# Kernel tuning notes

Hardware: AMD Instinct MI355X
Metric: run time of the kernel (lower is better)

Reference implementation:

```python
import jax, jax.numpy as jnp
import numpy as np

N_NODES = 100000
N_EDGES = 1600000
IN_DIM = 256
HIDDEN = 128
N_CLASSES = 40


def gcn_conv(x, W, b, src, dst, n_nodes):
    """torch_geometric GCNConv: transform -> add self-loops -> sym-normalized sum-aggregate -> +bias."""
    h = x @ W  # [N, out]
    loop = jnp.arange(n_nodes, dtype=src.dtype)
    src2 = jnp.concatenate([src, loop])
    dst2 = jnp.concatenate([dst, loop])
    # degree with self-loops (edge weight 1)
    deg = jax.ops.segment_sum(jnp.ones_like(dst2, dtype=h.dtype), dst2, num_segments=n_nodes)
    dinv = jnp.where(deg > 0, jax.lax.rsqrt(deg), 0.0)
    norm = dinv[src2] * dinv[dst2]  # [E+N]
    msg = h[src2] * norm[:, None]   # [E+N, out] gather + scale
    out = jax.ops.segment_sum(msg, dst2, num_segments=n_nodes)
    return out + b


def setup_inputs() -> dict:
    key = jax.random.key(0)
    k1, k2, k3, k4 = jax.random.split(key, 4)
    x = jax.random.normal(k1, (N_NODES, IN_DIM), dtype=jnp.float32)
    edge_index = jax.random.randint(k2, (2, N_EDGES), 0, N_NODES, dtype=jnp.int64)
    W1 = jax.random.normal(k3, (IN_DIM, HIDDEN), dtype=jnp.float32) * (1.0 / np.sqrt(IN_DIM))
    b1 = jnp.zeros((HIDDEN,), dtype=jnp.float32)
    W2 = jax.random.normal(k4, (HIDDEN, N_CLASSES), dtype=jnp.float32) * (1.0 / np.sqrt(HIDDEN))
    b2 = jnp.zeros((N_CLASSES,), dtype=jnp.float32)
    return {"x": x, "edge_index": edge_index, "W1": W1, "b1": b1, "W2": W2, "b2": b2}


def reference(x, edge_index, W1, b1, W2, b2):
    src, dst = edge_index[0], edge_index[1]
    h = gcn_conv(x, W1, b1, src, dst, N_NODES)
    h = jax.nn.relu(h)
    # dropout p=0.5 is identity in eval mode
    out = gcn_conv(h, W2, b2, src, dst, N_NODES)
    return out
```

## Files before the change

### kernel.cpp

```cpp
#include <hip/hip_runtime.h>
#include <hip/hip_bf16.h>
#include <hip/hip_fp16.h>

#define N_NODES 100000
#define N_EDGES 1600000
#define IN_DIM 256
#define HIDDEN 128
#define NCLS 40
#define NCLS_PAD 48

#define N_BUCKETS 256
#define NPB 391
#define BCAP 8192
#define EPT 16
#define BIN_WG 4096
#define BIN_BLOCKS 391
#define GEMM1_BLOCKS 782

typedef __attribute__((ext_vector_type(8))) _Float16 half8;
typedef __attribute__((ext_vector_type(4))) _Float16 half4f;
typedef __attribute__((ext_vector_type(4))) float floatx4;


__global__ __launch_bounds__(256) void k_prep(const float* __restrict__ W1, __half* __restrict__ W1T,
                                              const float* __restrict__ W2, __half* __restrict__ W2T,
                                              int* __restrict__ bfill) {
    const int t = threadIdx.x;
    if (blockIdx.x < 128) {
        int i = blockIdx.x * 256 + t;
        int k = i >> 7, n = i & 127;
        W1T[n * IN_DIM + k] = __float2half_rn(W1[i]);
    } else if (blockIdx.x == 128) {
        for (int i = t; i < NCLS_PAD * HIDDEN; i += 256) {
            int n = i >> 7, k = i & 127;
            W2T[n * HIDDEN + k] = (n < NCLS) ? __float2half_rn(W2[k * NCLS + n]) : __float2half_rn(0.f);
        }
    } else {
        bfill[t] = 0;
    }
}


__global__ __launch_bounds__(256) void k_binmm(const int* __restrict__ src, const int* __restrict__ dst,
                                               int* __restrict__ bfill,
                                               unsigned long long* __restrict__ bpair,
                                               const float* __restrict__ X,
                                               const __half* __restrict__ W1T,
                                               __half* __restrict__ H1s) {
    __shared__ __align__(16) char smraw[39936];
    const int t = threadIdx.x;

    if (blockIdx.x < BIN_BLOCKS) {
        int* hist   = (int*)smraw;
        int* bstart = hist + 256;
        int* gbase  = bstart + 256;
        unsigned long long* stage = (unsigned long long*)(smraw + 3072);
        unsigned char* bid = (unsigned char*)(smraw + 3072 + 32768);
        hist[t] = 0;
        __syncthreads();
        const long e0 = (long)blockIdx.x * BIN_WG;
        const int n_valid = (int)min((long)BIN_WG, (long)N_EDGES - e0);
        int msrc[EPT], mdst[EPT], moff[EPT];
        #pragma unroll
        for (int i = 0; i < EPT; i++) {
            long e = e0 + t + i * 256;
            if (e < N_EDGES) {
                msrc[i] = src[e];
                mdst[i] = dst[e];
                moff[i] = atomicAdd(&hist[mdst[i] / NPB], 1);
            } else {
                mdst[i] = -1;
            }
        }
        __syncthreads();
        if (t < 64) {
            int carry = 0;
            #pragma unroll
            for (int c = 0; c < 4; c++) {
                int idx = c * 64 + t;
                int hv = hist[idx];
                int s = hv;
                #pragma unroll
                for (int d2 = 1; d2 < 64; d2 <<= 1) {
                    int u = __shfl_up(s, d2, 64);
                    if (t >= d2) s += u;
                }
                bstart[idx] = carry + (s - hv);
                carry += __shfl(s, 63, 64);
            }
        }
        __syncthreads();
        int h = hist[t];
        gbase[t] = (h > 0) ? atomicAdd(&bfill[t], h) : 0;
        #pragma unroll
        for (int i = 0; i < EPT; i++) {
            if (mdst[i] >= 0) {
                int b = mdst[i] / NPB;
                int pos = bstart[b] + moff[i];
                stage[pos] = ((unsigned long long)(unsigned)mdst[i] << 32) | (unsigned)msrc[i];
                bid[pos] = (unsigned char)b;
            }
        }
        __syncthreads();
        for (int i = t; i < n_valid; i += 256) {
            int b = bid[i];
            int dest = gbase[b] + (i - bstart[b]);
            bpair[(long)b * BCAP + dest] = stage[i];
        }
        return;
    }

    _Float16 (*Asm)[72] = (_Float16(*)[72])smraw;
    _Float16 (*Bsm)[72] = (_Float16(*)[72])(smraw + 128 * 72 * 2);
    const int wave = t >> 6;
    const int lane = t & 63;
    const int m16  = lane & 15;
    const int kq   = lane >> 4;
    const int row0 = (blockIdx.x - BIN_BLOCKS) * 128;

    floatx4 acc[2][8];
    #pragma unroll
    for (int mt = 0; mt < 2; mt++)
        #pragma unroll
        for (int i = 0; i < 8; i++) acc[mt][i] = (floatx4)0.f;

    float4 ar[4][2];
    auto loadA = [&](int kcL) {
        #pragma unroll
        for (int it = 0; it < 4; it++) {
            int u = t + it * 256;
            int r = u >> 3, j = u & 7;
            int gr = row0 + r;
            if (gr < N_NODES) {
                const float* p = &X[(long)gr * IN_DIM + kcL * 64 + j * 8];
                ar[it][0] = *(const float4*)p;
                ar[it][1] = *(const float4*)(p + 4);
            } else {
                ar[it][0] = make_float4(0.f, 0.f, 0.f, 0.f);
                ar[it][1] = make_float4(0.f, 0.f, 0.f, 0.f);
            }
        }
    };

    loadA(0);
    for (int kc = 0; kc < 4; kc++) {
        #pragma unroll
        for (int it = 0; it < 4; it++) {
            int u = t + it * 256;
            int r = u >> 3, j = u & 7;
            half8 hh;
            hh[0] = (_Float16)ar[it][0].x; hh[1] = (_Float16)ar[it][0].y;
            hh[2] = (_Float16)ar[it][0].z; hh[3] = (_Float16)ar[it][0].w;
            hh[4] = (_Float16)ar[it][1].x; hh[5] = (_Float16)ar[it][1].y;
            hh[6] = (_Float16)ar[it][1].z; hh[7] = (_Float16)ar[it][1].w;
            *(half8*)&Asm[r][j * 8] = hh;
        }
        #pragma unroll
        for (int it = 0; it < 4; it++) {
            int u = t + it * 256;
            int n = u >> 3, j = u & 7;
            float4 w = *(const float4*)&W1T[n * IN_DIM + kc * 64 + j * 8];
            *(float4*)&Bsm[n][j * 8] = w;
        }
        __syncthreads();
        if (kc < 3) loadA(kc + 1);
        #pragma unroll
        for (int ks = 0; ks < 2; ks++) {
            half8 a0 = *(const half8*)&Asm[wave * 32 + m16][ks * 32 + kq * 8];
            half8 a1 = *(const half8*)&Asm[wave * 32 + 16 + m16][ks * 32 + kq * 8];
            #pragma unroll
            for (int nt = 0; nt < 8; nt++) {
                half8 b = *(const half8*)&Bsm[nt * 16 + m16][ks * 32 + kq * 8];
                acc[0][nt] = __builtin_amdgcn_mfma_f32_16x16x32_f16(a0, b, acc[0][nt], 0, 0, 0);
                acc[1][nt] = __builtin_amdgcn_mfma_f32_16x16x32_f16(a1, b, acc[1][nt], 0, 0, 0);
            }
        }
        __syncthreads();
    }
    #pragma unroll
    for (int mt = 0; mt < 2; mt++) {
        const int gr0 = row0 + wave * 32 + mt * 16 + kq * 4;
        #pragma unroll
        for (int nt = 0; nt < 8; nt++) {
            int c = nt * 16 + m16;
            #pragma unroll
            for (int r = 0; r < 4; r++) {
                if (gr0 + r < N_NODES)
                    H1s[(long)(gr0 + r) * HIDDEN + c] = __float2half_rn(acc[mt][nt][r]);
            }
        }
    }
}


__global__ __launch_bounds__(256) void k_build(const int* __restrict__ bfill,
                                               const unsigned long long* __restrict__ bpair,
                                               int* __restrict__ row_ptr, float* __restrict__ dinv,
                                               int* __restrict__ col) {
    __shared__ int h[NPB];
    __shared__ int pfx[NPB];
    __shared__ int sred[4];
    const int b  = blockIdx.x;
    const int nb = b * NPB;
    const int nn = min(NPB, N_NODES - nb);
    const int t  = threadIdx.x;
    int v = (t < b) ? bfill[t] : 0;
    #pragma unroll
    for (int dl = 32; dl > 0; dl >>= 1) v += __shfl_down(v, dl, 64);
    if ((t & 63) == 0) sred[t >> 6] = v;
    for (int i = t; i < NPB; i += 256) h[i] = 0;
    __syncthreads();
    const int base_b = sred[0] + sred[1] + sred[2] + sred[3];
    const int n = bfill[b];
    for (int i = t; i < n; i += 256) {
        int dd = (int)(bpair[(long)b * BCAP + i] >> 32);
        atomicAdd(&h[dd - nb], 1);
    }
    __syncthreads();
    if (t < 64) {
        int carry = 0;
        #pragma unroll
        for (int c = 0; c < (NPB + 63) / 64; c++) {
            int idx = c * 64 + t;
            int hv = (idx < nn) ? h[idx] : 0;
            int s = hv;
            #pragma unroll
            for (int d2 = 1; d2 < 64; d2 <<= 1) {
                int u = __shfl_up(s, d2, 64);
                if (t >= d2) s += u;
            }
            if (idx < nn) {
                int ex = base_b + carry + (s - hv);
                pfx[idx] = ex;
                row_ptr[nb + idx] = ex;
                dinv[nb + idx] = rsqrtf((float)(hv + 1));
            }
            carry += __shfl(s, 63, 64);
        }
    }
    __syncthreads();
    for (int i = t; i < nn; i += 256) h[i] = 0;
    __syncthreads();
    for (int i = t; i < n; i += 256) {
        unsigned long long p = bpair[(long)b * BCAP + i];
        int dd = (int)(p >> 32);
        int ss = (int)(p & 0xFFFFFFFFu);
        int pos = pfx[dd - nb] + atomicAdd(&h[dd - nb], 1);
        col[pos] = ss;
    }
    if (b == 0 && t == 0) row_ptr[N_NODES] = N_EDGES;
}


__global__ __launch_bounds__(256) void k_agg1g2(const __half* __restrict__ H1s,
                                                const int* __restrict__ row_ptr,
                                                const int* __restrict__ col,
                                                const float* __restrict__ dinv,
                                                const float* __restrict__ b1,
                                                const __half* __restrict__ W2T,
                                                __half* __restrict__ H2s) {
    __shared__ __align__(16) _Float16 rows[16][136];
    const int wave = threadIdx.x >> 6;
    const int lane = threadIdx.x & 63;
    const __half2* base = (const __half2*)H1s;
    const float2 bb = ((const float2*)b1)[lane];
    const int d00 = blockIdx.x * 16 + wave * 4;

    #pragma unroll
    for (int i = 0; i < 4; i++) {
        const int d = d00 + i;
        const int e0 = __builtin_amdgcn_readfirstlane(row_ptr[d]);
        const int e1 = __builtin_amdgcn_readfirstlane(row_ptr[d + 1]);
        const float dd = dinv[d];
        float ax = 0.f, ay = 0.f;
        int e = e0;
        for (; e + 7 < e1; e += 8) {
            int s0 = col[e],     s1 = col[e + 1], s2 = col[e + 2], s3 = col[e + 3];
            int s4 = col[e + 4], s5 = col[e + 5], s6 = col[e + 6], s7 = col[e + 7];
            float d0 = dinv[s0], d1 = dinv[s1], d2 = dinv[s2], d3 = dinv[s3];
            float d4 = dinv[s4], d5 = dinv[s5], d6 = dinv[s6], d7 = dinv[s7];
            float2 f0 = __half22float2(base[(long)s0 * 64 + lane]);
            float2 f1 = __half22float2(base[(long)s1 * 64 + lane]);
            float2 f2 = __half22float2(base[(long)s2 * 64 + lane]);
            float2 f3 = __half22float2(base[(long)s3 * 64 + lane]);
            float2 f4 = __half22float2(base[(long)s4 * 64 + lane]);
            float2 f5 = __half22float2(base[(long)s5 * 64 + lane]);
            float2 f6 = __half22float2(base[(long)s6 * 64 + lane]);
            float2 f7 = __half22float2(base[(long)s7 * 64 + lane]);
            ax += d0 * f0.x + d1 * f1.x + d2 * f2.x + d3 * f3.x
                + d4 * f4.x + d5 * f5.x + d6 * f6.x + d7 * f7.x;
            ay += d0 * f0.y + d1 * f1.y + d2 * f2.y + d3 * f3.y
                + d4 * f4.y + d5 * f5.y + d6 * f6.y + d7 * f7.y;
        }
        for (; e + 3 < e1; e += 4) {
            int s0 = col[e], s1 = col[e + 1], s2 = col[e + 2], s3 = col[e + 3];
            float d0 = dinv[s0], d1 = dinv[s1], d2 = dinv[s2], d3 = dinv[s3];
            float2 f0 = __half22float2(base[(long)s0 * 64 + lane]);
            float2 f1 = __half22float2(base[(long)s1 * 64 + lane]);
            float2 f2 = __half22float2(base[(long)s2 * 64 + lane]);
            float2 f3 = __half22float2(base[(long)s3 * 64 + lane]);
            ax += d0 * f0.x + d1 * f1.x + d2 * f2.x + d3 * f3.x;
            ay += d0 * f0.y + d1 * f1.y + d2 * f2.y + d3 * f3.y;
        }
        for (; e < e1; e++) {
            int s = col[e];
            float dv = dinv[s];
            float2 f = __half22float2(base[(long)s * 64 + lane]);
            ax += dv * f.x; ay += dv * f.y;
        }
        float2 fs = __half22float2(base[(long)d * 64 + lane]);
        ax += dd * fs.x; ay += dd * fs.y;
        float ox = fmaxf(dd * ax + bb.x, 0.f) * dd;
        float oy = fmaxf(dd * ay + bb.y, 0.f) * dd;
        *(__half2*)&rows[wave * 4 + i][lane * 2] =
            __halves2half2(__float2half_rn(ox), __float2half_rn(oy));
    }
    __syncthreads();

    if (wave < 3) {
        const int m16 = lane & 15;
        const int kq  = lane >> 4;
        floatx4 acc = (floatx4)0.f;
        #pragma unroll
        for (int ks = 0; ks < 4; ks++) {
            half8 a = *(const half8*)&rows[m16][ks * 32 + kq * 8];
            half8 b = *(const half8*)&W2T[(wave * 16 + m16) * HIDDEN + ks * 32 + kq * 8];
            acc = __builtin_amdgcn_mfma_f32_16x16x32_f16(a, b, acc, 0, 0, 0);
        }
        const int c = wave * 16 + m16;
        if (c < NCLS) {
            const int gr0 = blockIdx.x * 16 + kq * 4;
            #pragma unroll
            for (int r = 0; r < 4; r++)
                H2s[(long)(gr0 + r) * NCLS + c] = __float2half_rn(acc[r]);
        }
    }
}


__global__ __launch_bounds__(256) void k_agg2(const __half* __restrict__ H2s,
                                              const int* __restrict__ row_ptr,
                                              const int* __restrict__ col,
                                              const float* __restrict__ dinv,
                                              const float* __restrict__ b2,
                                              float* __restrict__ out) {
    const int wave = threadIdx.x >> 6;
    const int lane = threadIdx.x & 63;
    const int g = lane / 10;
    const int f = lane - g * 10;
    const int d = blockIdx.x * 24 + wave * 6 + g;
    const bool act = (g < 6) && (d < N_NODES);
    int e0 = 0, e1 = 0;
    if (act) { e0 = row_ptr[d]; e1 = row_ptr[d + 1]; }
    const half4f* base4 = (const half4f*)H2s;
    float s0 = 0.f, s1 = 0.f, s2 = 0.f, s3 = 0.f;
    int e = e0;
    while (__any(e < e1)) {
        #pragma unroll
        for (int u = 0; u < 4; u++) {
            if (e + u < e1) {
                half4f v = base4[(long)col[e + u] * 10 + f];
                s0 += (float)v[0]; s1 += (float)v[1]; s2 += (float)v[2]; s3 += (float)v[3];
            }
        }
        e += 4;
    }
    if (act) {
        half4f v = base4[(long)d * 10 + f];
        s0 += (float)v[0]; s1 += (float)v[1]; s2 += (float)v[2]; s3 += (float)v[3];
        float dd = dinv[d];
        float4 bbv = ((const float4*)b2)[f];
        float4 o = make_float4(dd * s0 + bbv.x, dd * s1 + bbv.y, dd * s2 + bbv.z, dd * s3 + bbv.w);
        ((float4*)out)[(long)d * 10 + f] = o;
    }
}


extern "C" void kernel_launch(void* const* d_in, const int* in_sizes, int n_in,
                              void* d_out, int out_size, void* d_ws, size_t ws_size,
                              hipStream_t stream) {
    const float* x  = (const float*)d_in[0];
    const int*   ei = (const int*)d_in[1];
    const float* W1 = (const float*)d_in[2];
    const float* b1 = (const float*)d_in[3];
    const float* W2 = (const float*)d_in[4];
    const float* b2 = (const float*)d_in[5];
    const int* srcE = ei;
    const int* dstE = ei + N_EDGES;

    int*   row_ptr = (int*)d_ws;
    int*   bfill   = row_ptr + 100032;
    int*   col     = bfill + 256;
    float* dinv    = (float*)(col + N_EDGES);
    __half* H1s    = (__half*)(dinv + 100032);
    __half* H2s    = H1s + (long)N_NODES * HIDDEN;
    __half* W1T    = H2s + (long)N_NODES * NCLS;
    __half* W2T    = W1T + IN_DIM * HIDDEN;
    unsigned long long* bpair = (unsigned long long*)(W2T + NCLS_PAD * HIDDEN);

    k_prep   <<<130, 256, 0, stream>>>(W1, W1T, W2, W2T, bfill);
    k_binmm  <<<BIN_BLOCKS + GEMM1_BLOCKS, 256, 0, stream>>>(srcE, dstE, bfill, bpair, x, W1T, H1s);
    k_build  <<<N_BUCKETS, 256, 0, stream>>>(bfill, bpair, row_ptr, dinv, col);
    k_agg1g2 <<<N_NODES / 16, 256, 0, stream>>>(H1s, row_ptr, col, dinv, b1, W2T, H2s);
    k_agg2   <<<(N_NODES + 23) / 24, 256, 0, stream>>>(H2s, row_ptr, col, dinv, b2, (float*)d_out);
}
```

Measured before the change: 337.9 us.

## Load GEMM operands directly from global into registers and interleave bin/GEMM blocks

```diff
diff --git a/kernel.cpp b/kernel.cpp
--- a/kernel.cpp
+++ b/kernel.cpp
@@ -12,9 +12,9 @@
 #define N_BUCKETS 256
 #define NPB 391
 #define BCAP 8192
-#define EPT 16
-#define BIN_WG 4096
-#define BIN_BLOCKS 391
+#define EPT 8
+#define BIN_WG 2048
+#define BIN_BLOCKS 782
 #define GEMM1_BLOCKS 782
 
 typedef __attribute__((ext_vector_type(8))) _Float16 half8;
@@ -41,24 +41,25 @@
 }
 
 
-__global__ __launch_bounds__(256) void k_binmm(const int* __restrict__ src, const int* __restrict__ dst,
-                                               int* __restrict__ bfill,
-                                               unsigned long long* __restrict__ bpair,
-                                               const float* __restrict__ X,
-                                               const __half* __restrict__ W1T,
-                                               __half* __restrict__ H1s) {
-    __shared__ __align__(16) char smraw[39936];
+__global__ __launch_bounds__(256, 4) void k_binmm(const int* __restrict__ src, const int* __restrict__ dst,
+                                                  int* __restrict__ bfill,
+                                                  unsigned long long* __restrict__ bpair,
+                                                  const float* __restrict__ X,
+                                                  const __half* __restrict__ W1T,
+                                                  __half* __restrict__ H1s) {
+    __shared__ __align__(16) char smraw[21504];
     const int t = threadIdx.x;
-
-    if (blockIdx.x < BIN_BLOCKS) {
+    const int half_id = blockIdx.x >> 1;
+
+    if ((blockIdx.x & 1) == 0) {
         int* hist   = (int*)smraw;
         int* bstart = hist + 256;
         int* gbase  = bstart + 256;
         unsigned long long* stage = (unsigned long long*)(smraw + 3072);
-        unsigned char* bid = (unsigned char*)(smraw + 3072 + 32768);
+        unsigned char* bid = (unsigned char*)(smraw + 3072 + 16384);
         hist[t] = 0;
         __syncthreads();
-        const long e0 = (long)blockIdx.x * BIN_WG;
+        const long e0 = (long)half_id * BIN_WG;
         const int n_valid = (int)min((long)BIN_WG, (long)N_EDGES - e0);
         int msrc[EPT], mdst[EPT], moff[EPT];
         #pragma unroll
@@ -110,13 +111,19 @@
         return;
     }
 
-    _Float16 (*Asm)[72] = (_Float16(*)[72])smraw;
-    _Float16 (*Bsm)[72] = (_Float16(*)[72])(smraw + 128 * 72 * 2);
     const int wave = t >> 6;
     const int lane = t & 63;
     const int m16  = lane & 15;
     const int kq   = lane >> 4;
-    const int row0 = (blockIdx.x - BIN_BLOCKS) * 128;
+    const int row0 = half_id * 128;
+    const int arow0 = row0 + wave * 32 + m16;
+    const int arow1 = arow0 + 16;
+    const bool va0 = arow0 < N_NODES;
+    const bool va1 = arow1 < N_NODES;
+    const float* pX0 = X + (long)arow0 * IN_DIM + kq * 8;
+    const float* pX1 = X + (long)arow1 * IN_DIM + kq * 8;
+    const __half* pB0 = W1T + m16 * IN_DIM + kq * 8;
+    const float4 z4 = make_float4(0.f, 0.f, 0.f, 0.f);
 
     floatx4 acc[2][8];
     #pragma unroll
@@ -124,59 +131,45 @@
         #pragma unroll
         for (int i = 0; i < 8; i++) acc[mt][i] = (floatx4)0.f;
 
-    float4 ar[4][2];
-    auto loadA = [&](int kcL) {
-        #pragma unroll
-        for (int it = 0; it < 4; it++) {
-            int u = t + it * 256;
-            int r = u >> 3, j = u & 7;
-            int gr = row0 + r;
-            if (gr < N_NODES) {
-                const float* p = &X[(long)gr * IN_DIM + kcL * 64 + j * 8];
-                ar[it][0] = *(const float4*)p;
-                ar[it][1] = *(const float4*)(p + 4);
-            } else {
-                ar[it][0] = make_float4(0.f, 0.f, 0.f, 0.f);
-                ar[it][1] = make_float4(0.f, 0.f, 0.f, 0.f);
-            }
-        }
-    };
-
-    loadA(0);
-    for (int kc = 0; kc < 4; kc++) {
-        #pragma unroll
-        for (int it = 0; it < 4; it++) {
-            int u = t + it * 256;
-            int r = u >> 3, j = u & 7;
-            half8 hh;
-            hh[0] = (_Float16)ar[it][0].x; hh[1] = (_Float16)ar[it][0].y;
-            hh[2] = (_Float16)ar[it][0].z; hh[3] = (_Float16)ar[it][0].w;
-            hh[4] = (_Float16)ar[it][1].x; hh[5] = (_Float16)ar[it][1].y;
-            hh[6] = (_Float16)ar[it][1].z; hh[7] = (_Float16)ar[it][1].w;
-            *(half8*)&Asm[r][j * 8] = hh;
-        }
-        #pragma unroll
-        for (int it = 0; it < 4; it++) {
-            int u = t + it * 256;
-            int n = u >> 3, j = u & 7;
-            float4 w = *(const float4*)&W1T[n * IN_DIM + kc * 64 + j * 8];
-            *(float4*)&Bsm[n][j * 8] = w;
-        }
-        __syncthreads();
-        if (kc < 3) loadA(kc + 1);
-        #pragma unroll
-        for (int ks = 0; ks < 2; ks++) {
-            half8 a0 = *(const half8*)&Asm[wave * 32 + m16][ks * 32 + kq * 8];
-            half8 a1 = *(const half8*)&Asm[wave * 32 + 16 + m16][ks * 32 + kq * 8];
-            #pragma unroll
-            for (int nt = 0; nt < 8; nt++) {
-                half8 b = *(const half8*)&Bsm[nt * 16 + m16][ks * 32 + kq * 8];
-                acc[0][nt] = __builtin_amdgcn_mfma_f32_16x16x32_f16(a0, b, acc[0][nt], 0, 0, 0);
-                acc[1][nt] = __builtin_amdgcn_mfma_f32_16x16x32_f16(a1, b, acc[1][nt], 0, 0, 0);
-            }
-        }
-        __syncthreads();
-    }
+    float4 curA[2][2], nxtA[2][2];
+    if (va0) { curA[0][0] = *(const float4*)pX0; curA[0][1] = *(const float4*)(pX0 + 4); }
+    else     { curA[0][0] = z4; curA[0][1] = z4; }
+    if (va1) { curA[1][0] = *(const float4*)pX1; curA[1][1] = *(const float4*)(pX1 + 4); }
+    else     { curA[1][0] = z4; curA[1][1] = z4; }
+
+    #pragma unroll
+    for (int s = 0; s < 8; s++) {
+        if (s < 7) {
+            const float* q0 = pX0 + (s + 1) * 32;
+            const float* q1 = pX1 + (s + 1) * 32;
+            if (va0) { nxtA[0][0] = *(const float4*)q0; nxtA[0][1] = *(const float4*)(q0 + 4); }
+            else     { nxtA[0][0] = z4; nxtA[0][1] = z4; }
+            if (va1) { nxtA[1][0] = *(const float4*)q1; nxtA[1][1] = *(const float4*)(q1 + 4); }
+            else     { nxtA[1][0] = z4; nxtA[1][1] = z4; }
+        }
+        half8 a0, a1;
+        a0[0] = (_Float16)curA[0][0].x; a0[1] = (_Float16)curA[0][0].y;
+        a0[2] = (_Float16)curA[0][0].z; a0[3] = (_Float16)curA[0][0].w;
+        a0[4] = (_Float16)curA[0][1].x; a0[5] = (_Float16)curA[0][1].y;
+        a0[6] = (_Float16)curA[0][1].z; a0[7] = (_Float16)curA[0][1].w;
+        a1[0] = (_Float16)curA[1][0].x; a1[1] = (_Float16)curA[1][0].y;
+        a1[2] = (_Float16)curA[1][0].z; a1[3] = (_Float16)curA[1][0].w;
+        a1[4] = (_Float16)curA[1][1].x; a1[5] = (_Float16)curA[1][1].y;
+        a1[6] = (_Float16)curA[1][1].z; a1[7] = (_Float16)curA[1][1].w;
+        const __half* pB = pB0 + s * 32;
+        #pragma unroll
+        for (int nt = 0; nt < 8; nt++) {
+            half8 b = *(const half8*)(pB + nt * 16 * IN_DIM);
+            acc[0][nt] = __builtin_amdgcn_mfma_f32_16x16x32_f16(a0, b, acc[0][nt], 0, 0, 0);
+            acc[1][nt] = __builtin_amdgcn_mfma_f32_16x16x32_f16(a1, b, acc[1][nt], 0, 0, 0);
+        }
+        #pragma unroll
+        for (int p = 0; p < 2; p++) {
+            curA[p][0] = nxtA[p][0];
+            curA[p][1] = nxtA[p][1];
+        }
+    }
+
     #pragma unroll
     for (int mt = 0; mt < 2; mt++) {
         const int gr0 = row0 + wave * 32 + mt * 16 + kq * 4;
```

After: 369.1 us. 9.2% more time.

## Double bucket count for CSR build, prefetch W1 tiles, unroll agg2 deeper

Applied to the files above, without the earlier changes.

```diff
diff --git a/kernel.cpp b/kernel.cpp
--- a/kernel.cpp
+++ b/kernel.cpp
@@ -9,9 +9,9 @@
 #define NCLS 40
 #define NCLS_PAD 48
 
-#define N_BUCKETS 256
-#define NPB 391
-#define BCAP 8192
+#define N_BUCKETS 512
+#define NPB 196
+#define BCAP 4096
 #define EPT 16
 #define BIN_WG 4096
 #define BIN_BLOCKS 391
@@ -37,6 +37,7 @@
         }
     } else {
         bfill[t] = 0;
+        bfill[t + 256] = 0;
     }
 }
 
@@ -47,16 +48,15 @@
                                                const float* __restrict__ X,
                                                const __half* __restrict__ W1T,
                                                __half* __restrict__ H1s) {
-    __shared__ __align__(16) char smraw[39936];
+    __shared__ __align__(16) char smraw[38912];
     const int t = threadIdx.x;
 
     if (blockIdx.x < BIN_BLOCKS) {
         int* hist   = (int*)smraw;
-        int* bstart = hist + 256;
-        int* gbase  = bstart + 256;
-        unsigned long long* stage = (unsigned long long*)(smraw + 3072);
-        unsigned char* bid = (unsigned char*)(smraw + 3072 + 32768);
-        hist[t] = 0;
+        int* bstart = hist + 512;
+        int* gbase  = bstart + 512;
+        unsigned long long* stage = (unsigned long long*)(smraw + 6144);
+        hist[t] = 0; hist[t + 256] = 0;
         __syncthreads();
         const long e0 = (long)blockIdx.x * BIN_WG;
         const int n_valid = (int)min((long)BIN_WG, (long)N_EDGES - e0);
@@ -76,7 +76,7 @@
         if (t < 64) {
             int carry = 0;
             #pragma unroll
-            for (int c = 0; c < 4; c++) {
+            for (int c = 0; c < 8; c++) {
                 int idx = c * 64 + t;
                 int hv = hist[idx];
                 int s = hv;
@@ -90,22 +90,24 @@
             }
         }
         __syncthreads();
-        int h = hist[t];
-        gbase[t] = (h > 0) ? atomicAdd(&bfill[t], h) : 0;
+        int h0 = hist[t], h1 = hist[t + 256];
+        gbase[t]       = (h0 > 0) ? atomicAdd(&bfill[t],       h0) : 0;
+        gbase[t + 256] = (h1 > 0) ? atomicAdd(&bfill[t + 256], h1) : 0;
         #pragma unroll
         for (int i = 0; i < EPT; i++) {
             if (mdst[i] >= 0) {
                 int b = mdst[i] / NPB;
                 int pos = bstart[b] + moff[i];
                 stage[pos] = ((unsigned long long)(unsigned)mdst[i] << 32) | (unsigned)msrc[i];
-                bid[pos] = (unsigned char)b;
             }
         }
         __syncthreads();
         for (int i = t; i < n_valid; i += 256) {
-            int b = bid[i];
+            unsigned long long p = stage[i];
+            int dd = (int)(p >> 32);
+            int b = dd / NPB;
             int dest = gbase[b] + (i - bstart[b]);
-            bpair[(long)b * BCAP + dest] = stage[i];
+            bpair[(long)b * BCAP + dest] = p;
         }
         return;
     }
@@ -125,6 +127,7 @@
         for (int i = 0; i < 8; i++) acc[mt][i] = (floatx4)0.f;
 
     float4 ar[4][2];
+    float4 br[4];
     auto loadA = [&](int kcL) {
         #pragma unroll
         for (int it = 0; it < 4; it++) {
@@ -141,8 +144,16 @@
             }
         }
     };
-
-    loadA(0);
+    auto loadB = [&](int kcL) {
+        #pragma unroll
+        for (int it = 0; it < 4; it++) {
+            int u = t + it * 256;
+            int n = u >> 3, j = u & 7;
+            br[it] = *(const float4*)&W1T[n * IN_DIM + kcL * 64 + j * 8];
+        }
+    };
+
+    loadA(0); loadB(0);
     for (int kc = 0; kc < 4; kc++) {
         #pragma unroll
         for (int it = 0; it < 4; it++) {
@@ -159,11 +170,10 @@
         for (int it = 0; it < 4; it++) {
             int u = t + it * 256;
             int n = u >> 3, j = u & 7;
-            float4 w = *(const float4*)&W1T[n * IN_DIM + kc * 64 + j * 8];
-            *(float4*)&Bsm[n][j * 8] = w;
-        }
-        __syncthreads();
-        if (kc < 3) loadA(kc + 1);
+            *(float4*)&Bsm[n][j * 8] = br[it];
+        }
+        __syncthreads();
+        if (kc < 3) { loadA(kc + 1); loadB(kc + 1); }
         #pragma unroll
         for (int ks = 0; ks < 2; ks++) {
             half8 a0 = *(const half8*)&Asm[wave * 32 + m16][ks * 32 + kq * 8];
@@ -204,7 +214,9 @@
     const int nb = b * NPB;
     const int nn = min(NPB, N_NODES - nb);
     const int t  = threadIdx.x;
-    int v = (t < b) ? bfill[t] : 0;
+    int v = 0;
+    if (t < b) v += bfill[t];
+    if (t + 256 < b) v += bfill[t + 256];
     #pragma unroll
     for (int dl = 32; dl > 0; dl >>= 1) v += __shfl_down(v, dl, 64);
     if ((t & 63) == 0) sred[t >> 6] = v;
@@ -357,13 +369,13 @@
     int e = e0;
     while (__any(e < e1)) {
         #pragma unroll
-        for (int u = 0; u < 4; u++) {
+        for (int u = 0; u < 8; u++) {
             if (e + u < e1) {
                 half4f v = base4[(long)col[e + u] * 10 + f];
                 s0 += (float)v[0]; s1 += (float)v[1]; s2 += (float)v[2]; s3 += (float)v[3];
             }
         }
-        e += 4;
+        e += 8;
     }
     if (act) {
         half4f v = base4[(long)d * 10 + f];
@@ -390,7 +402,7 @@
 
     int*   row_ptr = (int*)d_ws;
     int*   bfill   = row_ptr + 100032;
-    int*   col     = bfill + 256;
+    int*   col     = bfill + 512;
     float* dinv    = (float*)(col + N_EDGES);
     __half* H1s    = (__half*)(dinv + 100032);
     __half* H2s    = H1s + (long)N_NODES * HIDDEN;
```

Result: no change. 341.9 us (+1.2%).
